# Performance work log

Hardware: AMD Instinct MI355X
Metric: run time of the kernel (lower is better)

Reference implementation:

```python
import jax, jax.numpy as jnp
import numpy as np

B, REP = 32, 1024
N_VERBS, N_ROLES, N_NOUNS, MR = 504, 190, 11538, 6
HID, NHEADS, MAXN = 32, 4, 512


def setup_inputs() -> dict:
    key = jax.random.key(0)
    ks = jax.random.split(key, 16)
    s = 0.05  # weight scale
    return {
        "rep": jax.random.normal(ks[0], (B, REP), jnp.float32),
        "W_v": jax.random.normal(ks[1], (REP, N_VERBS), jnp.float32) * s,
        "b_v": jax.random.normal(ks[2], (N_VERBS,), jnp.float32) * s,
        "W_r": jax.random.normal(ks[3], (REP, N_ROLES * HID), jnp.float32) * s,
        "b_r": jax.random.normal(ks[4], (N_ROLES * HID,), jnp.float32) * s,
        "attn_in_w": jax.random.normal(ks[5], (3, 3 * HID, HID), jnp.float32) * s,
        "attn_in_b": jax.random.normal(ks[6], (3, 3 * HID), jnp.float32) * s,
        "attn_out_w": jax.random.normal(ks[7], (3, HID, HID), jnp.float32) * s,
        "attn_out_b": jax.random.normal(ks[8], (3, HID), jnp.float32) * s,
        "W_n": jax.random.normal(ks[9], (HID, N_NOUNS), jnp.float32) * s,
        "b_n": jax.random.normal(ks[10], (N_NOUNS,), jnp.float32) * s,
        "r_n_idx": jax.random.randint(ks[11], (N_ROLES, MAXN), 0, N_NOUNS, jnp.int32),
        "pad_v_r": jax.random.randint(ks[12], (N_VERBS, MR), 0, N_ROLES + 1, jnp.int32),
    }


def _mha(x, in_w, in_b, out_w, out_b):
    # x: [L, B, E] self-attention, torch nn.MultiheadAttention semantics
    L, Bn, E = x.shape
    hd = E // NHEADS
    qkv = x @ in_w.T + in_b                      # [L, B, 3E]
    q, k, v = jnp.split(qkv, 3, axis=-1)
    q = q.reshape(L, Bn, NHEADS, hd)
    k = k.reshape(L, Bn, NHEADS, hd)
    v = v.reshape(L, Bn, NHEADS, hd)
    scores = jnp.einsum("lbhd,mbhd->bhlm", q, k) / jnp.sqrt(jnp.float32(hd))
    attn = jax.nn.softmax(scores, axis=-1)
    out = jnp.einsum("bhlm,mbhd->lbhd", attn, v).reshape(L, Bn, E)
    return out @ out_w.T + out_b


def reference(rep, W_v, b_v, W_r, b_r, attn_in_w, attn_in_b, attn_out_w,
              attn_out_b, W_n, b_n, r_n_idx, pad_v_r):
    batch = rep.shape[0]
    v_potential = rep @ W_v + b_v                          # [B, V]
    node = (rep @ W_r + b_r).reshape(batch, N_ROLES, HID)
    node = jnp.transpose(node, (1, 0, 2))                  # [R, B, H]
    for i in range(3):
        node = _mha(node, attn_in_w[i], attn_in_b[i], attn_out_w[i], attn_out_b[i])
    rn_potential = node @ W_n + b_n                        # [R, B, N_nouns]

    # grouped index_select per role: [R, B, MAXN]
    grouped = jax.vmap(lambda pot, idx: pot[:, idx])(rn_potential, r_n_idx)
    r_max = grouped.max(axis=-1)                           # [R, B]
    maxi = grouped.argmax(axis=-1)                         # [R, B]
    rn_marginal = r_max + jnp.log(jnp.exp(grouped - r_max[..., None]).sum(-1))
    r_maxi = jax.vmap(lambda idx, mi: idx[mi])(r_n_idx, maxi)  # global noun ids

    # [B, R] then prepend the zero/padding column -> [B, 1+R]
    zeros_f = jnp.zeros((batch, 1), rn_marginal.dtype)
    zeros_i = jnp.zeros((batch, 1), r_maxi.dtype)
    rn_marginal = jnp.concatenate([zeros_f, rn_marginal.T], axis=1)
    r_max = jnp.concatenate([zeros_f, r_max.T], axis=1)
    r_maxi = jnp.concatenate([zeros_i, r_maxi.T], axis=1)

    # gather per-verb role groups: [B, V, MR]
    vrn_marginal_g = rn_marginal[:, pad_v_r]
    vr_max_g = r_max[:, pad_v_r]
    vr_maxi_g = r_maxi[:, pad_v_r]

    v_marginal = vrn_marginal_g.sum(2) + v_potential       # [B, V]
    m = v_marginal.max(1)
    norm = m + jnp.log(jnp.exp(v_marginal - m[:, None]).sum(1))
    v_max = vr_max_g.sum(2) + v_potential                  # [B, V]
    return (rep, v_potential, rn_potential, norm, v_max, vr_maxi_g)
```

## Files before the change

### kernel.cpp

```cpp
#include <hip/hip_runtime.h>
#include <math.h>

#define B_    32
#define REP_  1024
#define NV_   504
#define NR_   190
#define NN_   11538
#define MR_   6
#define HID_  32
#define NH_   4
#define HD_   8
#define MAXN_ 512

#define O_VP   32768
#define O_RN   48896
#define O_NORM 70199936
#define O_VMAX 70199968
#define O_MAXI 70216096

#define W_REPT  0
#define W_WT    32768
#define W_PN    401984
#define W_PV    1958464
#define W_N0    2087488
#define W_HOB   2282048
#define W_HOA   2476608
#define W_MARG  2671168
#define W_RMAX  2677248
#define W_RMAXI 2683328
#define W_WC    2689408

__global__ __launch_bounds__(256) void k_tr_rep(const float* __restrict__ rep,
                                                float* __restrict__ repT) {
    int gid = blockIdx.x * 256 + threadIdx.x;
    int b = gid & 31, k = gid >> 5;
    repT[gid] = rep[b * REP_ + k];
}

__global__ __launch_bounds__(256) void k_pre(const float* __restrict__ Wn,
                                             float* __restrict__ Wt,
                                             const float* __restrict__ ainw,
                                             const float* __restrict__ ainb,
                                             const float* __restrict__ aoutw,
                                             const float* __restrict__ aoutb,
                                             float* __restrict__ wc) {
    __shared__ float t[32][33];
    int tid = threadIdx.x;
    if (blockIdx.x < 361) {
        int n0 = blockIdx.x * 32;
        #pragma unroll
        for (int p = 0; p < 4; p++) {
            int idx = p * 256 + tid;
            int k = idx >> 5, n = idx & 31;
            int nn = n0 + n;
            t[k][n] = (nn < NN_) ? Wn[(size_t)k * NN_ + nn] : 0.f;
        }
        __syncthreads();
        #pragma unroll
        for (int p = 0; p < 4; p++) {
            int idx = p * 256 + tid;
            int n = idx >> 5, k = idx & 31;
            int nn = n0 + n;
            if (nn < NN_) Wt[nn * 32 + k] = t[k][n];
        }
    } else {
        #pragma unroll 1
        for (int layer = 0; layer < 2; layer++) {
            const float* iw  = ainw + (layer + 1) * 3072;
            const float* ib  = ainb + (layer + 1) * 96;
            const float* ow  = aoutw + layer * 1024;
            const float* obv = aoutb + layer * 32;
            float* W = wc + layer * 3168;
            for (int idx = tid; idx < 3072; idx += 256) {
                int row = idx >> 5, d = idx & 31;
                float s = 0.f;
                #pragma unroll
                for (int e = 0; e < 32; e++) s += iw[row * 32 + e] * ow[e * 32 + d];
                W[idx] = s;
            }
            if (tid < 96) {
                float s = ib[tid];
                #pragma unroll
                for (int e = 0; e < 32; e++) s += iw[tid * 32 + e] * obv[e];
                W[3072 + tid] = s;
            }
        }
    }
}

__global__ __launch_bounds__(256) void k_gemm(const float* __restrict__ Wr,
                                              const float* __restrict__ Wv,
                                              const float4* __restrict__ repT4,
                                              float* __restrict__ pn,
                                              float* __restrict__ pv) {
    int bx = blockIdx.x;
    int lane = threadIdx.x & 63;
    int bg = threadIdx.x >> 6;
    int k0 = blockIdx.y * 128;
    int rbase = k0 * 8 + bg * 2;
    float acc[8] = {0.f,0.f,0.f,0.f,0.f,0.f,0.f,0.f};
    if (bx < 95) {
        int c = bx * 64 + lane;
        const float* w = Wr + (size_t)k0 * 6080 + c;
        #pragma unroll 4
        for (int k = 0; k < 128; k++) {
            float wv = w[(size_t)k * 6080];
            float4 ra = repT4[rbase + k * 8];
            float4 rb = repT4[rbase + k * 8 + 1];
            acc[0] += ra.x * wv; acc[1] += ra.y * wv; acc[2] += ra.z * wv; acc[3] += ra.w * wv;
            acc[4] += rb.x * wv; acc[5] += rb.y * wv; acc[6] += rb.z * wv; acc[7] += rb.w * wv;
        }
        size_t base = (size_t)blockIdx.y * 194560 + (size_t)(bg * 8) * 6080 + c;
        #pragma unroll
        for (int i = 0; i < 8; i++) pn[base + (size_t)i * 6080] = acc[i];
    } else {
        int c = (bx - 95) * 64 + lane;
        if (c >= NV_) return;
        const float* w = Wv + (size_t)k0 * NV_ + c;
        #pragma unroll 4
        for (int k = 0; k < 128; k++) {
            float wv = w[(size_t)k * NV_];
            float4 ra = repT4[rbase + k * 8];
            float4 rb = repT4[rbase + k * 8 + 1];
            acc[0] += ra.x * wv; acc[1] += ra.y * wv; acc[2] += ra.z * wv; acc[3] += ra.w * wv;
            acc[4] += rb.x * wv; acc[5] += rb.y * wv; acc[6] += rb.z * wv; acc[7] += rb.w * wv;
        }
        size_t base = (size_t)blockIdx.y * 16128 + (size_t)(bg * 8) * NV_ + c;
        #pragma unroll
        for (int i = 0; i < 8; i++) pv[base + (size_t)i * NV_] = acc[i];
    }
}

__global__ __launch_bounds__(256) void k_reduce(const float* __restrict__ pn,
                                                const float* __restrict__ pv,
                                                const float* __restrict__ br,
                                                const float* __restrict__ bv,
                                                float* __restrict__ node0,
                                                float* __restrict__ vpot) {
    int bid = blockIdx.x, tid = threadIdx.x;
    if (bid < 760) {
        int gid = bid * 256 + tid;
        int b = gid / 6080, c = gid - b * 6080;
        float s = br[c];
        #pragma unroll
        for (int kz = 0; kz < 8; kz++) s += pn[kz * 194560 + gid];
        node0[(c >> 5) * 1024 + b * 32 + (c & 31)] = s;
    } else {
        int gid = (bid - 760) * 256 + tid;
        int v = gid % NV_;
        float s = bv[v];
        #pragma unroll
        for (int kz = 0; kz < 8; kz++) s += pv[kz * 16128 + gid];
        vpot[gid] = s;
    }
}

__global__ __launch_bounds__(256) void k_attn(const float* __restrict__ xin,
                                              const float* __restrict__ winw,
                                              const float* __restrict__ winb,
                                              float* __restrict__ ho) {
    int b = blockIdx.x >> 2, h = blockIdx.x & 3;
    int tid = threadIdx.x;
    __shared__ __align__(16) float qs[192 * 12];
    __shared__ __align__(16) float ks[192 * 12];
    __shared__ __align__(16) float vs[192 * 12];
    __shared__ __align__(16) float pmS[4 * 192];
    __shared__ __align__(16) float psS[4 * 192];
    __shared__ __align__(16) float poS[4 * 192 * 8];

    if (tid < NR_) {
        const float* xr = xin + tid * 1024 + b * 32;
        float4 xv[8];
        #pragma unroll
        for (int q = 0; q < 8; q++) xv[q] = *(const float4*)(xr + q * 4);
        #pragma unroll 1
        for (int part = 0; part < 3; part++) {
            float* dst = (part == 0) ? qs : (part == 1) ? ks : vs;
            #pragma unroll 1
            for (int jj = 0; jj < 8; jj++) {
                int row = part * 32 + h * 8 + jj;
                const float* wr = winw + row * 32;
                float s = winb[row];
                #pragma unroll
                for (int q = 0; q < 8; q++) {
                    s += xv[q].x * wr[q*4+0] + xv[q].y * wr[q*4+1] +
                         xv[q].z * wr[q*4+2] + xv[q].w * wr[q*4+3];
                }
                dst[tid * 12 + jj] = s;
            }
        }
    }
    __syncthreads();

    int wave = tid >> 6, lane = tid & 63;
    int m0 = wave * 48;
    int m1 = (m0 + 48 < NR_) ? (m0 + 48) : NR_;
    float4 qa[3], qb[3];
    #pragma unroll
    for (int i = 0; i < 3; i++) {
        int l = lane + 64 * i;
        if (l < NR_) {
            qa[i] = *(const float4*)&qs[l * 12];
            qb[i] = *(const float4*)&qs[l * 12 + 4];
        } else {
            qa[i] = make_float4(0.f,0.f,0.f,0.f);
            qb[i] = make_float4(0.f,0.f,0.f,0.f);
        }
    }
    float mM[3] = {-INFINITY, -INFINITY, -INFINITY};
    float sS[3] = {0.f, 0.f, 0.f};
    float o[3][8];
    #pragma unroll
    for (int i = 0; i < 3; i++)
        #pragma unroll
        for (int d = 0; d < 8; d++) o[i][d] = 0.f;
    const float scale = 0.3535533905932738f;
    for (int mm = m0; mm < m1; mm++) {
        float4 ka = *(const float4*)&ks[mm * 12];
        float4 kb = *(const float4*)&ks[mm * 12 + 4];
        float4 va = *(const float4*)&vs[mm * 12];
        float4 vb = *(const float4*)&vs[mm * 12 + 4];
        #pragma unroll
        for (int i = 0; i < 3; i++) {
            float sc = (qa[i].x*ka.x + qa[i].y*ka.y + qa[i].z*ka.z + qa[i].w*ka.w +
                        qb[i].x*kb.x + qb[i].y*kb.y + qb[i].z*kb.z + qb[i].w*kb.w) * scale;
            if (sc > mM[i]) {
                float al = __expf(mM[i] - sc);
                sS[i] = sS[i] * al + 1.f;
                mM[i] = sc;
                o[i][0] = o[i][0]*al + va.x; o[i][1] = o[i][1]*al + va.y;
                o[i][2] = o[i][2]*al + va.z; o[i][3] = o[i][3]*al + va.w;
                o[i][4] = o[i][4]*al + vb.x; o[i][5] = o[i][5]*al + vb.y;
                o[i][6] = o[i][6]*al + vb.z; o[i][7] = o[i][7]*al + vb.w;
            } else {
                float p = __expf(sc - mM[i]);
                sS[i] += p;
                o[i][0] += p*va.x; o[i][1] += p*va.y; o[i][2] += p*va.z; o[i][3] += p*va.w;
                o[i][4] += p*vb.x; o[i][5] += p*vb.y; o[i][6] += p*vb.z; o[i][7] += p*vb.w;
            }
        }
    }
    #pragma unroll
    for (int i = 0; i < 3; i++) {
        int slot = wave * 192 + lane + 64 * i;
        pmS[slot] = mM[i];
        psS[slot] = sS[i];
        *(float4*)&poS[slot * 8]     = make_float4(o[i][0], o[i][1], o[i][2], o[i][3]);
        *(float4*)&poS[slot * 8 + 4] = make_float4(o[i][4], o[i][5], o[i][6], o[i][7]);
    }
    __syncthreads();

    if (tid < NR_) {
        float M = pmS[tid], S = psS[tid];
        float4 oa = *(const float4*)&poS[tid * 8];
        float4 ob = *(const float4*)&poS[tid * 8 + 4];
        #pragma unroll
        for (int w = 1; w < 4; w++) {
            int slot = w * 192 + tid;
            float m2 = pmS[slot], s2 = psS[slot];
            float4 pa = *(const float4*)&poS[slot * 8];
            float4 pb = *(const float4*)&poS[slot * 8 + 4];
            if (m2 > M) {
                float al = __expf(M - m2);
                S = S * al + s2;
                oa.x = oa.x*al + pa.x; oa.y = oa.y*al + pa.y; oa.z = oa.z*al + pa.z; oa.w = oa.w*al + pa.w;
                ob.x = ob.x*al + pb.x; ob.y = ob.y*al + pb.y; ob.z = ob.z*al + pb.z; ob.w = ob.w*al + pb.w;
                M = m2;
            } else {
                float p = __expf(m2 - M);
                S += s2 * p;
                oa.x += p*pa.x; oa.y += p*pa.y; oa.z += p*pa.z; oa.w += p*pa.w;
                ob.x += p*pb.x; ob.y += p*pb.y; ob.z += p*pb.z; ob.w += p*pb.w;
            }
        }
        float inv = 1.f / S;
        float* hp = ho + tid * 1024 + b * 32 + h * 8;
        *(float4*)hp       = make_float4(oa.x*inv, oa.y*inv, oa.z*inv, oa.w*inv);
        *(float4*)(hp + 4) = make_float4(ob.x*inv, ob.y*inv, ob.z*inv, ob.w*inv);
    }
}

__global__ __launch_bounds__(256, 4) void k_big(const float* __restrict__ ho3,
                                                const float* __restrict__ ow3,
                                                const float* __restrict__ ob3,
                                                const float* __restrict__ Wn,
                                                const float* __restrict__ bn,
                                                const float* __restrict__ Wt,
                                                const int* __restrict__ rni,
                                                float* __restrict__ out_rn,
                                                float* __restrict__ marg,
                                                float* __restrict__ rmax,
                                                int* __restrict__ rmaxi) {
    int bid = blockIdx.x;
    int tid = threadIdx.x;
    __shared__ __align__(16) float smem[8192 + 2048 + 1024 + 32];
    float* Ws  = smem;
    float* Ask = smem + 8192;
    float* ows = smem + 10240;
    float* obs = smem + 11264;

    for (int i = tid; i < 1024; i += 256) ows[i] = ow3[i];
    if (tid < 32) obs[tid] = ob3[tid];

    if (bid >= 190) {
        int g  = bid - 190;
        int bx = g % 95;
        int by = g / 95;
        int t0 = bx * 64;
        int c0 = by * 256;
        bool tail = (c0 + 256 > NN_);

        #pragma unroll
        for (int p = 0; p < 16; p++) {
            int idx = p * 256 + tid;
            int k  = idx >> 7;
            int c2 = (idx & 127) * 2;
            int cg = c0 + c2;
            float2 v = (cg < NN_) ? *(const float2*)&Wn[(size_t)k * NN_ + cg]
                                  : make_float2(0.f, 0.f);
            *(float2*)&Ws[k * 256 + c2] = v;
        }
        __syncthreads();

        {
            int r = tid >> 2, hq = tid & 3;
            const float4* hp = (const float4*)&ho3[(size_t)(t0 + r) * 32];
            float4 hv[8];
            #pragma unroll
            for (int q = 0; q < 8; q++) hv[q] = hp[q];
            #pragma unroll
            for (int i = 0; i < 8; i++) {
                int h = hq * 8 + i;
                float s = obs[h];
                #pragma unroll
                for (int d4 = 0; d4 < 8; d4++) {
                    float4 h4 = hv[d4];
                    float4 w = *(const float4*)&ows[h * 32 + d4 * 4];
                    s += h4.x*w.x + h4.y*w.y + h4.z*w.z + h4.w*w.w;
                }
                Ask[h * 64 + r] = s;
            }
        }
        __syncthreads();

        int wave = tid >> 6, lane = tid & 63;
        int r0 = wave * 16;
        int cL = lane * 4;
        int c  = c0 + cL;
        float acc[16][4];
        #pragma unroll
        for (int r = 0; r < 16; r++)
            #pragma unroll
            for (int q = 0; q < 4; q++) acc[r][q] = 0.f;

        #pragma unroll 4
        for (int k = 0; k < 32; k++) {
            float4 wv = *(const float4*)&Ws[k * 256 + cL];
            float4 av[4];
            av[0] = *(const float4*)&Ask[k * 64 + r0];
            av[1] = *(const float4*)&Ask[k * 64 + r0 + 4];
            av[2] = *(const float4*)&Ask[k * 64 + r0 + 8];
            av[3] = *(const float4*)&Ask[k * 64 + r0 + 12];
            const float* ap = (const float*)av;
            #pragma unroll
            for (int r = 0; r < 16; r++) {
                float a = ap[r];
                acc[r][0] += a * wv.x; acc[r][1] += a * wv.y;
                acc[r][2] += a * wv.z; acc[r][3] += a * wv.w;
            }
        }

        if (!tail) {
            float4 bb = *(const float4*)&bn[c];
            #pragma unroll
            for (int r = 0; r < 16; r++) {
                size_t base = (size_t)(t0 + r0 + r) * NN_ + c;
                float v0 = acc[r][0] + bb.x, v1 = acc[r][1] + bb.y;
                float v2 = acc[r][2] + bb.z, v3 = acc[r][3] + bb.w;
                if ((r & 1) == 0) {
                    *(float4*)&out_rn[base] = make_float4(v0, v1, v2, v3);
                } else {
                    *(float2*)&out_rn[base]     = make_float2(v0, v1);
                    *(float2*)&out_rn[base + 2] = make_float2(v2, v3);
                }
            }
        } else {
            #pragma unroll
            for (int r = 0; r < 16; r++) {
                size_t base = (size_t)(t0 + r0 + r) * NN_;
                #pragma unroll
                for (int q = 0; q < 4; q++) {
                    if (c + q < NN_)
                        out_rn[base + c + q] = acc[r][q] + bn[c + q];
                }
            }
        }
    } else {
        int l = bid;
        int jg = tid >> 5, b = tid & 31;
        float* pm   = smem;
        float* psum = smem + 256;
        int*   pj   = (int*)(smem + 512);
        float4 hv[8];
        {
            const float4* hp = (const float4*)&ho3[(size_t)l * 1024 + b * 32];
            #pragma unroll
            for (int q = 0; q < 8; q++) hv[q] = hp[q];
        }
        __syncthreads();
        float4 nd[8];
        #pragma unroll
        for (int q = 0; q < 8; q++) {
            float s[4];
            #pragma unroll
            for (int j = 0; j < 4; j++) {
                int h = q * 4 + j;
                float a = obs[h];
                #pragma unroll
                for (int d4 = 0; d4 < 8; d4++) {
                    float4 h4 = hv[d4];
                    float4 w = *(const float4*)&ows[h * 32 + d4 * 4];
                    a += h4.x*w.x + h4.y*w.y + h4.z*w.z + h4.w*w.w;
                }
                s[j] = a;
            }
            nd[q] = make_float4(s[0], s[1], s[2], s[3]);
        }
        float lm = -INFINITY, ls = 0.f;
        int jm = 0;
        const int* ip = &rni[l * 512];
        for (int jj = 0; jj < 64; jj++) {
            int j = jg * 64 + jj;
            int idx = ip[j];
            const float4* wr = (const float4*)&Wt[idx * 32];
            float s = bn[idx];
            #pragma unroll
            for (int q = 0; q < 8; q++) {
                float4 w4 = wr[q];
                s += nd[q].x*w4.x + nd[q].y*w4.y + nd[q].z*w4.z + nd[q].w*w4.w;
            }
            if (s > lm) { ls = ls * __expf(lm - s) + 1.f; lm = s; jm = j; }
            else        { ls += __expf(s - lm); }
        }
        pm[b * 8 + jg] = lm; psum[b * 8 + jg] = ls; pj[b * 8 + jg] = jm;
        __syncthreads();
        if (tid < 32) {
            int bb = tid;
            float M = pm[bb * 8], S = psum[bb * 8];
            int J = pj[bb * 8];
            for (int i = 1; i < 8; i++) {
                float m2 = pm[bb * 8 + i], s2 = psum[bb * 8 + i];
                if (m2 > M) { S = S * __expf(M - m2) + s2; M = m2; J = pj[bb * 8 + i]; }
                else        { S += s2 * __expf(m2 - M); }
            }
            int t = l * 32 + bb;
            marg[t]  = M + logf(S);
            rmax[t]  = M;
            rmaxi[t] = ip[J];
        }
    }
}

__global__ __launch_bounds__(256) void k_final(const float* __restrict__ marg,
                                               const float* __restrict__ rmax,
                                               const int* __restrict__ rmaxi,
                                               const int* __restrict__ pad,
                                               const float* __restrict__ vpot,
                                               float* __restrict__ out_norm,
                                               float* __restrict__ out_vmax,
                                               float* __restrict__ out_maxi) {
    int b = blockIdx.x, tid = threadIdx.x;
    __shared__ float me[191], xe[191];
    __shared__ int ie[191];
    __shared__ float vm[NV_];
    __shared__ float rbuf[4];
    if (tid < 191) {
        if (tid == 0) { me[0] = 0.f; xe[0] = 0.f; ie[0] = 0; }
        else {
            int t = (tid - 1) * 32 + b;
            me[tid] = marg[t]; xe[tid] = rmax[t]; ie[tid] = rmaxi[t];
        }
    }
    __syncthreads();
    for (int v = tid; v < NV_; v += 256) {
        float sm = 0.f, sx = 0.f;
        float vp = vpot[b * NV_ + v];
        #pragma unroll
        for (int i = 0; i < 6; i++) {
            int p = pad[v * 6 + i];
            sm += me[p]; sx += xe[p];
            out_maxi[(size_t)(b * NV_ + v) * 6 + i] = (float)ie[p];
        }
        vm[v] = sm + vp;
        out_vmax[b * NV_ + v] = sx + vp;
    }
    __syncthreads();
    float m = -INFINITY;
    for (int v = tid; v < NV_; v += 256) m = fmaxf(m, vm[v]);
    #pragma unroll
    for (int off = 32; off > 0; off >>= 1) m = fmaxf(m, __shfl_xor(m, off));
    if ((tid & 63) == 0) rbuf[tid >> 6] = m;
    __syncthreads();
    float M = fmaxf(fmaxf(rbuf[0], rbuf[1]), fmaxf(rbuf[2], rbuf[3]));
    __syncthreads();
    float s = 0.f;
    for (int v = tid; v < NV_; v += 256) s += __expf(vm[v] - M);
    #pragma unroll
    for (int off = 32; off > 0; off >>= 1) s += __shfl_xor(s, off);
    if ((tid & 63) == 0) rbuf[tid >> 6] = s;
    __syncthreads();
    if (tid == 0) out_norm[b] = M + logf(rbuf[0] + rbuf[1] + rbuf[2] + rbuf[3]);
}

extern "C" void kernel_launch(void* const* d_in, const int* in_sizes, int n_in,
                              void* d_out, int out_size, void* d_ws, size_t ws_size,
                              hipStream_t stream) {
    const float* rep   = (const float*)d_in[0];
    const float* Wv    = (const float*)d_in[1];
    const float* bv    = (const float*)d_in[2];
    const float* Wr    = (const float*)d_in[3];
    const float* br    = (const float*)d_in[4];
    const float* ainw  = (const float*)d_in[5];
    const float* ainb  = (const float*)d_in[6];
    const float* aoutw = (const float*)d_in[7];
    const float* aoutb = (const float*)d_in[8];
    const float* Wn    = (const float*)d_in[9];
    const float* bn    = (const float*)d_in[10];
    const int*   rni   = (const int*)d_in[11];
    const int*   pad   = (const int*)d_in[12];
    float* out = (float*)d_out;
    float* ws  = (float*)d_ws;

    float* repT = ws + W_REPT;
    float* Wt   = ws + W_WT;
    float* pn   = ws + W_PN;
    float* pv   = ws + W_PV;
    float* n0   = ws + W_N0;
    float* hoA  = ws + W_HOA;
    float* hoB  = ws + W_HOB;
    float* marg = ws + W_MARG;
    float* rmx  = ws + W_RMAX;
    int*   rmi  = (int*)(ws + W_RMAXI);
    float* wc   = ws + W_WC;

    hipMemcpyAsync(out, rep, 32768 * sizeof(float), hipMemcpyDeviceToDevice, stream);
    k_tr_rep<<<128, 256, 0, stream>>>(rep, repT);
    k_pre<<<362, 256, 0, stream>>>(Wn, Wt, ainw, ainb, aoutw, aoutb, wc);
    k_gemm<<<dim3(103, 8), 256, 0, stream>>>(Wr, Wv, (const float4*)repT, pn, pv);
    k_reduce<<<823, 256, 0, stream>>>(pn, pv, br, bv, n0, out + O_VP);

    k_attn<<<128, 256, 0, stream>>>(n0,  ainw,      ainb,      hoA);
    k_attn<<<128, 256, 0, stream>>>(hoA, wc,        wc + 3072, hoB);
    k_attn<<<128, 256, 0, stream>>>(hoB, wc + 3168, wc + 6240, hoA);

    k_big<<<190 + 95 * 46, 256, 0, stream>>>(hoA, aoutw + 2048, aoutb + 64,
                                             Wn, bn, Wt, rni,
                                             out + O_RN, marg, rmx, rmi);
    k_final<<<32, 256, 0, stream>>>(marg, rmx, rmi, pad, out + O_VP,
                                    out + O_NORM, out + O_VMAX, out + O_MAXI);
}
```

Baseline: 588.7 us.

## Halve k_big column tile, drop LDS weight staging, fold rep copy into k_pre

The dense noun-potential tiles in k_big shrink from 256 to 128 columns, which doubles the grid and halves the accumulator registers and LDS footprint per block to raise occupancy. The out-projection weights and bias are now read directly from global/constant cache instead of being staged in LDS. The per-block __syncthreads is removed from the role-max path. The rep transpose and the rep output copy are merged into extra blocks of k_pre, removing a memcpy and a kernel launch. Stores become float2-wide instead of float4, and the removed barrier after the Ws fill relies on the later barrier before the GEMM loop.

```diff
diff --git a/kernel.cpp b/kernel.cpp
--- a/kernel.cpp
+++ b/kernel.cpp
@@ -30,20 +30,16 @@
 #define W_RMAXI 2683328
 #define W_WC    2689408
 
-__global__ __launch_bounds__(256) void k_tr_rep(const float* __restrict__ rep,
-                                                float* __restrict__ repT) {
-    int gid = blockIdx.x * 256 + threadIdx.x;
-    int b = gid & 31, k = gid >> 5;
-    repT[gid] = rep[b * REP_ + k];
-}
-
 __global__ __launch_bounds__(256) void k_pre(const float* __restrict__ Wn,
                                              float* __restrict__ Wt,
                                              const float* __restrict__ ainw,
                                              const float* __restrict__ ainb,
                                              const float* __restrict__ aoutw,
                                              const float* __restrict__ aoutb,
-                                             float* __restrict__ wc) {
+                                             float* __restrict__ wc,
+                                             const float* __restrict__ rep,
+                                             float* __restrict__ repT,
+                                             float* __restrict__ out_rep) {
     __shared__ float t[32][33];
     int tid = threadIdx.x;
     if (blockIdx.x < 361) {
@@ -63,7 +59,7 @@
             int nn = n0 + n;
             if (nn < NN_) Wt[nn * 32 + k] = t[k][n];
         }
-    } else {
+    } else if (blockIdx.x == 361) {
         #pragma unroll 1
         for (int layer = 0; layer < 2; layer++) {
             const float* iw  = ainw + (layer + 1) * 3072;
@@ -85,6 +81,11 @@
                 W[3072 + tid] = s;
             }
         }
+    } else {
+        int gid = (blockIdx.x - 362) * 256 + tid;
+        int b = gid & 31, k = gid >> 5;
+        out_rep[gid] = rep[gid];
+        repT[gid]    = rep[b * REP_ + k];
     }
 }
 
@@ -293,34 +294,27 @@
                                                 int* __restrict__ rmaxi) {
     int bid = blockIdx.x;
     int tid = threadIdx.x;
-    __shared__ __align__(16) float smem[8192 + 2048 + 1024 + 32];
+    __shared__ __align__(16) float smem[4096 + 2048];
     float* Ws  = smem;
-    float* Ask = smem + 8192;
-    float* ows = smem + 10240;
-    float* obs = smem + 11264;
-
-    for (int i = tid; i < 1024; i += 256) ows[i] = ow3[i];
-    if (tid < 32) obs[tid] = ob3[tid];
+    float* Ask = smem + 4096;
 
     if (bid >= 190) {
         int g  = bid - 190;
         int bx = g % 95;
         int by = g / 95;
         int t0 = bx * 64;
-        int c0 = by * 256;
-        bool tail = (c0 + 256 > NN_);
-
-        #pragma unroll
-        for (int p = 0; p < 16; p++) {
+        int c0 = by * 128;
+
+        #pragma unroll
+        for (int p = 0; p < 8; p++) {
             int idx = p * 256 + tid;
-            int k  = idx >> 7;
-            int c2 = (idx & 127) * 2;
+            int k  = idx >> 6;
+            int c2 = (idx & 63) * 2;
             int cg = c0 + c2;
             float2 v = (cg < NN_) ? *(const float2*)&Wn[(size_t)k * NN_ + cg]
                                   : make_float2(0.f, 0.f);
-            *(float2*)&Ws[k * 256 + c2] = v;
-        }
-        __syncthreads();
+            *(float2*)&Ws[k * 128 + c2] = v;
+        }
 
         {
             int r = tid >> 2, hq = tid & 3;
@@ -331,11 +325,11 @@
             #pragma unroll
             for (int i = 0; i < 8; i++) {
                 int h = hq * 8 + i;
-                float s = obs[h];
+                float s = ob3[h];
                 #pragma unroll
                 for (int d4 = 0; d4 < 8; d4++) {
                     float4 h4 = hv[d4];
-                    float4 w = *(const float4*)&ows[h * 32 + d4 * 4];
+                    float4 w = *(const float4*)&ow3[h * 32 + d4 * 4];
                     s += h4.x*w.x + h4.y*w.y + h4.z*w.z + h4.w*w.w;
                 }
                 Ask[h * 64 + r] = s;
@@ -345,17 +339,15 @@
 
         int wave = tid >> 6, lane = tid & 63;
         int r0 = wave * 16;
-        int cL = lane * 4;
+        int cL = lane * 2;
         int c  = c0 + cL;
-        float acc[16][4];
-        #pragma unroll
-        for (int r = 0; r < 16; r++)
-            #pragma unroll
-            for (int q = 0; q < 4; q++) acc[r][q] = 0.f;
+        float acc[16][2];
+        #pragma unroll
+        for (int r = 0; r < 16; r++) { acc[r][0] = 0.f; acc[r][1] = 0.f; }
 
         #pragma unroll 4
         for (int k = 0; k < 32; k++) {
-            float4 wv = *(const float4*)&Ws[k * 256 + cL];
+            float2 wv = *(const float2*)&Ws[k * 128 + cL];
             float4 av[4];
             av[0] = *(const float4*)&Ask[k * 64 + r0];
             av[1] = *(const float4*)&Ask[k * 64 + r0 + 4];
@@ -365,34 +357,18 @@
             #pragma unroll
             for (int r = 0; r < 16; r++) {
                 float a = ap[r];
-                acc[r][0] += a * wv.x; acc[r][1] += a * wv.y;
-                acc[r][2] += a * wv.z; acc[r][3] += a * wv.w;
-            }
-        }
-
-        if (!tail) {
-            float4 bb = *(const float4*)&bn[c];
+                acc[r][0] += a * wv.x;
+                acc[r][1] += a * wv.y;
+            }
+        }
+
+        if (c < NN_) {
+            float2 bb = *(const float2*)&bn[c];
             #pragma unroll
             for (int r = 0; r < 16; r++) {
                 size_t base = (size_t)(t0 + r0 + r) * NN_ + c;
-                float v0 = acc[r][0] + bb.x, v1 = acc[r][1] + bb.y;
-                float v2 = acc[r][2] + bb.z, v3 = acc[r][3] + bb.w;
-                if ((r & 1) == 0) {
-                    *(float4*)&out_rn[base] = make_float4(v0, v1, v2, v3);
-                } else {
-                    *(float2*)&out_rn[base]     = make_float2(v0, v1);
-                    *(float2*)&out_rn[base + 2] = make_float2(v2, v3);
-                }
-            }
-        } else {
-            #pragma unroll
-            for (int r = 0; r < 16; r++) {
-                size_t base = (size_t)(t0 + r0 + r) * NN_;
-                #pragma unroll
-                for (int q = 0; q < 4; q++) {
-                    if (c + q < NN_)
-                        out_rn[base + c + q] = acc[r][q] + bn[c + q];
-                }
+                *(float2*)&out_rn[base] = make_float2(acc[r][0] + bb.x,
+                                                      acc[r][1] + bb.y);
             }
         }
     } else {
@@ -407,7 +383,6 @@
             #pragma unroll
             for (int q = 0; q < 8; q++) hv[q] = hp[q];
         }
-        __syncthreads();
         float4 nd[8];
         #pragma unroll
         for (int q = 0; q < 8; q++) {
@@ -415,11 +390,11 @@
             #pragma unroll
             for (int j = 0; j < 4; j++) {
                 int h = q * 4 + j;
-                float a = obs[h];
+                float a = ob3[h];
                 #pragma unroll
                 for (int d4 = 0; d4 < 8; d4++) {
                     float4 h4 = hv[d4];
-                    float4 w = *(const float4*)&ows[h * 32 + d4 * 4];
+                    float4 w = *(const float4*)&ow3[h * 32 + d4 * 4];
                     a += h4.x*w.x + h4.y*w.y + h4.z*w.z + h4.w*w.w;
                 }
                 s[j] = a;
@@ -543,9 +518,8 @@
     int*   rmi  = (int*)(ws + W_RMAXI);
     float* wc   = ws + W_WC;
 
-    hipMemcpyAsync(out, rep, 32768 * sizeof(float), hipMemcpyDeviceToDevice, stream);
-    k_tr_rep<<<128, 256, 0, stream>>>(rep, repT);
-    k_pre<<<362, 256, 0, stream>>>(Wn, Wt, ainw, ainb, aoutw, aoutb, wc);
+    k_pre<<<490, 256, 0, stream>>>(Wn, Wt, ainw, ainb, aoutw, aoutb, wc,
+                                   rep, repT, out);
     k_gemm<<<dim3(103, 8), 256, 0, stream>>>(Wr, Wv, (const float4*)repT, pn, pv);
     k_reduce<<<823, 256, 0, stream>>>(pn, pv, br, bv, n0, out + O_VP);
 
@@ -553,7 +527,7 @@
     k_attn<<<128, 256, 0, stream>>>(hoA, wc,        wc + 3072, hoB);
     k_attn<<<128, 256, 0, stream>>>(hoB, wc + 3168, wc + 6240, hoA);
 
-    k_big<<<190 + 95 * 46, 256, 0, stream>>>(hoA, aoutw + 2048, aoutb + 64,
+    k_big<<<190 + 95 * 91, 256, 0, stream>>>(hoA, aoutw + 2048, aoutb + 64,
                                              Wn, bn, Wt, rni,
                                              out + O_RN, marg, rmx, rmi);
     k_final<<<32, 256, 0, stream>>>(marg, rmx, rmi, pad, out + O_VP,
```

Measured after the change: 739.4 us. 25.6% more time.
